# Optimization experiments

Hardware: AMD Instinct MI355X
Metric: run time of the kernel (lower is better)

## Reference

```python
import jax, jax.numpy as jnp
import numpy as np

# ---- problem sizes (would come from edge_index / init args in the torch module) ----
N = 10000      # number of nodes
E = 100000     # number of edges
C = 6          # channels per node
L = 6          # layers
B = 16         # batch
N_IN = 100     # input nodes  (nodes [0, N_IN))
N_OUT = 100    # output nodes (nodes [N-N_OUT, N))
EPS = 1e-5


def setup_inputs() -> dict:
    rng = np.random.default_rng(0)
    src = rng.integers(0, N, size=E).astype(np.int32)
    dst = rng.integers(0, N, size=E).astype(np.int32)

    input_mask = np.zeros(N, bool); input_mask[:N_IN] = True
    output_mask = np.zeros(N, bool); output_mask[N - N_OUT:] = True
    func_mask = ~(input_mask | output_mask)
    func_nodes = np.nonzero(func_mask)[0].astype(np.int32)
    F = func_nodes.size
    ii = np.arange(C, dtype=np.int32)

    # W1 (E -> C*N): edge e feeds all C channels of its dst node. nnz = E*C
    w1_rows = np.repeat(np.arange(E, dtype=np.int32), C)
    w1_cols = (dst[:, None] * C + ii[None, :]).reshape(-1)

    # W2 (C*N -> C*N): dense CxC block per function node. nnz = F*C*C
    base = np.repeat(func_nodes * C, C * C)
    w2_rows = base + np.tile(np.repeat(ii, C), F)
    w2_cols = base + np.tile(np.tile(ii, C), F)

    # W3 (C*N -> E): edge e reads the C channels of src(e) if src is a function node
    e_sel = np.nonzero(func_mask[src])[0].astype(np.int32)
    w3_rows = (src[e_sel][:, None] * C + ii[None, :]).reshape(-1)
    w3_cols = np.repeat(e_sel, C)

    # values: kaiming-style init with fan d (d=C for W1/W2, d=1 for W3)
    w1_vals = (rng.standard_normal(w1_rows.size) / np.sqrt(C)).astype(np.float32)
    w2_vals = (rng.standard_normal(w2_rows.size) / np.sqrt(C)).astype(np.float32)
    w3_vals = (rng.standard_normal(w3_rows.size) * 1.0).astype(np.float32)

    key = jax.random.key(0)
    x = jax.random.normal(key, (B, N), dtype=jnp.float32)

    return {
        "x": x,
        "src": jnp.asarray(src), "dst": jnp.asarray(dst),
        "output_mask": jnp.asarray(output_mask),
        "w1_rows": jnp.asarray(w1_rows), "w1_cols": jnp.asarray(w1_cols),
        "w1_vals": jnp.asarray(w1_vals), "b1": jnp.zeros((C * N,), jnp.float32),
        "w2_rows": jnp.asarray(w2_rows), "w2_cols": jnp.asarray(w2_cols),
        "w2_vals": jnp.asarray(w2_vals), "b2": jnp.zeros((C * N,), jnp.float32),
        "w3_rows": jnp.asarray(w3_rows), "w3_cols": jnp.asarray(w3_cols),
        "w3_vals": jnp.asarray(w3_vals), "b3": jnp.zeros((E,), jnp.float32),
        "gamma": jnp.ones((L,), jnp.float32), "beta": jnp.zeros((L,), jnp.float32),
    }


def _sp_lin(h, rows, cols, vals, bias, out_dim):
    # out[b, c] = sum_{k: cols[k]==c} h[b, rows[k]] * vals[k] + bias[c]
    contrib = h[:, rows] * vals  # [B, nnz]
    out = jnp.zeros((h.shape[0], out_dim), h.dtype).at[:, cols].add(contrib)
    return out + bias


def _batchnorm_scalar(z, g, b):
    # BatchNorm1d(1) on z.view(-1,1): single channel over all B*E elements (training mode)
    m = jnp.mean(z)
    v = jnp.mean(jnp.square(z - m))
    return (z - m) * jax.lax.rsqrt(v + EPS) * g + b


def reference(x, src, dst, output_mask,
              w1_rows, w1_cols, w1_vals, b1,
              w2_rows, w2_cols, w2_vals, b2,
              w3_rows, w3_cols, w3_vals, b3,
              gamma, beta):
    x0 = x[:, src]          # node2edge: [B, E]
    h = x0
    h_last = x0             # residual=True path
    for l in range(L):
        z = _sp_lin(h, w1_rows, w1_cols, w1_vals, b1, C * N)
        z = jax.nn.elu(z)
        z = _sp_lin(z, w2_rows, w2_cols, w2_vals, b2, C * N)
        z = jax.nn.elu(z)
        z = _sp_lin(z, w3_rows, w3_cols, w3_vals, b3, E)
        z = _batchnorm_scalar(z, gamma[l], beta[l])
        h = z + h_last
        h_last = h
    h = h / L
    # edge2node: scatter edge values to dst nodes, keep only output nodes
    node = jnp.zeros((x.shape[0], N), x.dtype).at[:, dst].add(h)
    return jnp.where(output_mask[None, :], node, 0.0)
```

## Files before the change

kernel.cpp:

```cpp
#include <hip/hip_runtime.h>
#include <math.h>

#define NN 10000
#define NE 100000
#define CC 6
#define LL 6
#define BB 16
#define FUNC_LO 100
#define FUNC_HI 9900
#define NOUT 100
#define EPSF 1e-5f
#define NSLOT 64

struct Slot { double s1, s2; double pad[6]; };

struct Params {
  const float *x, *w1v, *b1, *w2v, *b2, *w3v, *b3, *gamma, *beta;
  const int *src, *dst, *w3r, *w3c;
  float *out;
  int *row_start, *counts, *fill, *slot;
  int *row2, *counts2, *fill2, *csr2;
  float4 *grec;
  float4 *srec;
  float *xT, *h;
  unsigned short *z3a, *z3b;
  float *A;
  float *Cw;
  Slot *part, *baseS;
  int F, Ksel;
};

__device__ __forceinline__ float eluf(float x){ return x > 0.0f ? x : expm1f(x); }
__device__ __forceinline__ float bf2f(unsigned short h){
  union { unsigned int u; float f; } c; c.u = ((unsigned int)h)<<16; return c.f;
}
__device__ __forceinline__ unsigned short f2bf(float f){
  union { float f; unsigned int u; } c; c.f = f;
  return (unsigned short)((c.u + 0x7FFFu + ((c.u>>16)&1u)) >> 16);
}

__device__ void block_add_slot(double a, double q, Slot* sl){
  __shared__ double sb1[4], sb2[4];
  #pragma unroll
  for(int off=32;off;off>>=1){ a+=__shfl_down(a,off); q+=__shfl_down(q,off); }
  int wid = threadIdx.x>>6;
  if((threadIdx.x&63)==0){ sb1[wid]=a; sb2[wid]=q; }
  __syncthreads();
  if(threadIdx.x==0){
    double A=sb1[0]+sb1[1]+sb1[2]+sb1[3];
    double Q=sb2[0]+sb2[1]+sb2[2]+sb2[3];
    if(A!=0.0) atomicAdd(&sl->s1,A);
    if(Q!=0.0) atomicAdd(&sl->s2,Q);
  }
  __syncthreads();
}

__device__ void bn_params(const Slot* part, const Slot* baseS, float* m, float* inv){
  __shared__ double s_mv[2];
  if(threadIdx.x < NSLOT){
    double a = part[threadIdx.x].s1 + baseS[threadIdx.x].s1;
    double q = part[threadIdx.x].s2 + baseS[threadIdx.x].s2;
    #pragma unroll
    for(int off=32;off;off>>=1){ a+=__shfl_down(a,off); q+=__shfl_down(q,off); }
    if(threadIdx.x==0){
      const double cnt = (double)NE*(double)BB;
      double md = a/cnt, vd = q/cnt - md*md;
      s_mv[0]=md; s_mv[1]=1.0/sqrt(vd+(double)EPSF);
    }
  }
  __syncthreads();
  *m=(float)s_mv[0]; *inv=(float)s_mv[1];
  __syncthreads();
}

__global__ __launch_bounds__(256) void kw_P1(Params p){
  int tid = blockIdx.x*256 + threadIdx.x, nt = gridDim.x*256;
  for(int i=tid;i<NN*BB;i+=nt){ int n=i>>4, b=i&15; p.xT[i]=p.x[b*NN+n]; }
  for(int i=tid;i<BB*NN;i+=nt) p.out[i]=0.f;
  double a=0.0,q=0.0;
  for(int e=tid;e<NE;e+=nt){
    atomicAdd(&p.counts[p.dst[e]],1);
    int s=p.src[e];
    if(!(s>=FUNC_LO && s<FUNC_HI)){ double v=(double)p.b3[e]; a+=v; q+=v*v; }
  }
  for(int k=tid;k<p.Ksel;k+=nt){
    int s=p.w3r[k*CC]/CC;
    atomicAdd(&p.counts2[s-FUNC_LO],1);
  }
  block_add_slot(a*BB, q*BB, &p.baseS[blockIdx.x&(NSLOT-1)]);
}

__global__ __launch_bounds__(256) void kw_scan(Params p){
  __shared__ int s_scan[256];
  const int*  cin  = (blockIdx.x==0)? p.counts : p.counts2;
  int*        rout = (blockIdx.x==0)? p.row_start : p.row2;
  const int   nel  = (blockIdx.x==0)? NN : p.F;
  const int   CH   = (nel+255)/256;
  int t=threadIdx.x, base=t*CH, s=0;
  for(int k=0;k<CH;k++){ int i=base+k; if(i<nel) s+=cin[i]; }
  s_scan[t]=s; __syncthreads();
  for(int off=1;off<256;off<<=1){
    int v=(t>=off)?s_scan[t-off]:0; __syncthreads();
    s_scan[t]+=v; __syncthreads();
  }
  int run=s_scan[t]-s;
  for(int k=0;k<CH;k++){ int i=base+k; if(i<nel){ rout[i]=run; run+=cin[i]; } }
  if(t==255) rout[nel]=s_scan[255];
}

__global__ __launch_bounds__(256) void kw_fill(Params p){
  int tid = blockIdx.x*256 + threadIdx.x, nt = gridDim.x*256;
  for(int e=tid;e<NE;e+=nt){
    int n=p.dst[e];
    int pos=p.row_start[n]+atomicAdd(&p.fill[n],1);
    p.slot[e]=pos;
    const float* w=&p.w1v[e*CC];
    int s=p.src[e];
    float b3v=p.b3[e];
    p.grec[pos*2  ]=make_float4(w[0],w[1],w[2],w[3]);
    p.grec[pos*2+1]=make_float4(w[4],w[5],__int_as_float(s),b3v);
    if(!(s>=FUNC_LO && s<FUNC_HI)){
      unsigned int hb = f2bf(b3v);
      unsigned int pk = hb | (hb<<16);
      uint4 v4 = make_uint4(pk,pk,pk,pk);
      uint4* za=(uint4*)&p.z3a[pos*BB];
      uint4* zb=(uint4*)&p.z3b[pos*BB];
      za[0]=v4; za[1]=v4; zb[0]=v4; zb[1]=v4;
    }
  }
  for(int k=tid;k<p.Ksel;k+=nt){
    int fi=p.w3r[k*CC]/CC - FUNC_LO;
    int pos=p.row2[fi]+atomicAdd(&p.fill2[fi],1);
    p.csr2[pos]=k;
  }
}

template<int MODE>
__global__ __launch_bounds__(256) void kw_AB(Params p, int l,
    const unsigned short* __restrict__ z3p, unsigned short* __restrict__ z3c){
  int tid = blockIdx.x*256 + (int)threadIdx.x, nt = gridDim.x*256;
  float c1=0.f, c2=0.f;
  if(MODE>0){
    float m, inv;
    bn_params(p.part+(l-1)*NSLOT, p.baseS, &m, &inv);
    float g=p.gamma[l-1], be=p.beta[l-1];
    c1 = inv*g; c2 = be - m*c1;
  }
  const int FB2 = p.F*32;
  double a=0.0, q=0.0;
  for(int t=tid;t<FB2;t+=nt){
    int fi = t>>5;
    int u  = t&31, b = u&15, half = u>>4;
    int n  = FUNC_LO+fi;
    float acc[CC], cacc[CC];
    #pragma unroll
    for(int i=0;i<CC;i++){ acc[i]=0.f; cacc[i]=0.f; }
    int beg=p.row_start[n], end=p.row_start[n+1];
    int pp = beg + half;
    for(; pp+2<end; pp+=4){
      float4 ra0=p.grec[pp*2],     rb0=p.grec[pp*2+1];
      float4 ra1=p.grec[(pp+2)*2], rb1=p.grec[(pp+2)*2+1];
      float hv0, hv1;
      if(MODE==0){
        int s0=__float_as_int(rb0.z), s1=__float_as_int(rb1.z);
        hv0 = p.xT[s0*BB+b];
        hv1 = p.xT[s1*BB+b];
        cacc[0]+=ra0.x+ra1.x; cacc[1]+=ra0.y+ra1.y; cacc[2]+=ra0.z+ra1.z;
        cacc[3]+=ra0.w+ra1.w; cacc[4]+=rb0.x+rb1.x; cacc[5]+=rb0.y+rb1.y;
      } else {
        hv0 = bf2f(z3p[pp*BB+b]);
        hv1 = bf2f(z3p[(pp+2)*BB+b]);
      }
      acc[0]+=hv0*ra0.x+hv1*ra1.x; acc[1]+=hv0*ra0.y+hv1*ra1.y;
      acc[2]+=hv0*ra0.z+hv1*ra1.z; acc[3]+=hv0*ra0.w+hv1*ra1.w;
      acc[4]+=hv0*rb0.x+hv1*rb1.x; acc[5]+=hv0*rb0.y+hv1*rb1.y;
    }
    if(pp<end){
      float4 ra0=p.grec[pp*2], rb0=p.grec[pp*2+1];
      float hv0;
      if(MODE==0){
        int s0=__float_as_int(rb0.z);
        hv0 = p.xT[s0*BB+b];
        cacc[0]+=ra0.x; cacc[1]+=ra0.y; cacc[2]+=ra0.z;
        cacc[3]+=ra0.w; cacc[4]+=rb0.x; cacc[5]+=rb0.y;
      } else {
        hv0 = bf2f(z3p[pp*BB+b]);
      }
      acc[0]+=hv0*ra0.x; acc[1]+=hv0*ra0.y; acc[2]+=hv0*ra0.z;
      acc[3]+=hv0*ra0.w; acc[4]+=hv0*rb0.x; acc[5]+=hv0*rb0.y;
    }
    float z1v[CC];
    #pragma unroll
    for(int i=0;i<CC;i++){
      acc[i] += __shfl_xor(acc[i],16);
      if(MODE==0){
        cacc[i] += __shfl_xor(cacc[i],16);
        if(half==0){
          p.A[(fi*CC+i)*BB+b] = acc[i];
          if(b==0) p.Cw[fi*CC+i] = cacc[i];
        }
        z1v[i] = eluf(acc[i] + p.b1[n*CC+i]);
      } else {
        float Aold = p.A[(fi*CC+i)*BB+b];
        float Cv   = p.Cw[fi*CC+i];
        float Anew = Aold + c1*acc[i] + c2*Cv;
        if(half==0) p.A[(fi*CC+i)*BB+b] = Anew;
        z1v[i] = eluf(Anew + p.b1[n*CC+i]);
      }
    }
    const float* W2=&p.w2v[fi*36];
    float z2[CC];
    #pragma unroll
    for(int jj=0;jj<CC;jj++){
      float o=p.b2[n*CC+jj];
      #pragma unroll
      for(int i=0;i<CC;i++) o+=z1v[i]*W2[i*CC+jj];
      z2[jj]=eluf(o);
    }
    int bg2=p.row2[fi], en2=p.row2[fi+1];
    if(MODE==0){
      for(int sp=bg2+half;sp<en2;sp+=2){
        int k=p.csr2[sp];
        int e=p.w3c[k*CC];
        const float* w=&p.w3v[k*CC];
        float b3v=p.b3[e];
        int sl=p.slot[e];
        if(b==0){
          p.srec[sp*2  ]=make_float4(w[0],w[1],w[2],w[3]);
          p.srec[sp*2+1]=make_float4(w[4],w[5],__int_as_float(sl),b3v);
        }
        float o = b3v + z2[0]*w[0]+z2[1]*w[1]+z2[2]*w[2]
                      + z2[3]*w[3]+z2[4]*w[4]+z2[5]*w[5];
        z3c[sl*BB+b]=f2bf(o);
        a+=o; q+=(double)o*o;
      }
    } else {
      for(int sp=bg2+half;sp<en2;sp+=2){
        float4 ra=p.srec[sp*2], rb=p.srec[sp*2+1];
        float o = rb.w + z2[0]*ra.x + z2[1]*ra.y + z2[2]*ra.z
                       + z2[3]*ra.w + z2[4]*rb.x + z2[5]*rb.y;
        int sl=__float_as_int(rb.z);
        z3c[sl*BB+b]=f2bf(o);
        a+=o; q+=(double)o*o;
      }
    }
  }
  if(MODE>0){
    int outBeg = p.row_start[FUNC_HI];
    int tot = (p.row_start[NN]-outBeg)*BB;
    for(int u=tid; u<tot; u+=nt){
      int pp=outBeg+(u>>4); int bb=u&15;
      float zb=bf2f(z3p[pp*BB+bb]);
      float hb;
      if(MODE==1){
        float4 rb=p.grec[pp*2+1];
        int s=__float_as_int(rb.z);
        hb=p.xT[s*BB+bb];
      } else {
        hb=p.h[pp*BB+bb];
      }
      p.h[pp*BB+bb]=hb+zb*c1+c2;
    }
  }
  block_add_slot(a,q,&p.part[l*NSLOT+(blockIdx.x&(NSLOT-1))]);
}

__global__ __launch_bounds__(256) void kw_out(Params p, const unsigned short* __restrict__ z3p){
  int tid = blockIdx.x*256 + threadIdx.x, nt = gridDim.x*256;
  float m,inv;
  bn_params(p.part+(LL-1)*NSLOT, p.baseS, &m, &inv);
  float g=p.gamma[LL-1], be=p.beta[LL-1];
  float c1=inv*g, c2=be-m*c1;
  for(int t=tid;t<NOUT*BB;t+=nt){
    int j=t>>4, b=t&15;
    int n=FUNC_HI+j;
    float acc=0.f;
    int beg=p.row_start[n], end=p.row_start[n+1];
    for(int pp=beg;pp<end;++pp){
      acc += p.h[pp*BB+b] + bf2f(z3p[pp*BB+b])*c1 + c2;
    }
    p.out[b*NN+n]=acc*(1.0f/(float)LL);
  }
}

extern "C" void kernel_launch(void* const* d_in, const int* in_sizes, int n_in,
                              void* d_out, int out_size, void* d_ws, size_t ws_size,
                              hipStream_t stream){
  Params p;
  p.x    =(const float*)d_in[0];
  p.src  =(const int*)  d_in[1];
  p.dst  =(const int*)  d_in[2];
  p.w1v  =(const float*)d_in[6];
  p.b1   =(const float*)d_in[7];
  p.w2v  =(const float*)d_in[10];
  p.b2   =(const float*)d_in[11];
  p.w3r  =(const int*)  d_in[12];
  p.w3c  =(const int*)  d_in[13];
  p.w3v  =(const float*)d_in[14];
  p.b3   =(const float*)d_in[15];
  p.gamma=(const float*)d_in[16];
  p.beta =(const float*)d_in[17];
  p.out  =(float*)d_out;
  p.F    = in_sizes[8]/36;
  p.Ksel = in_sizes[12]/CC;

  char* ws=(char*)d_ws; size_t off=0;
  auto alloc=[&](size_t bytes)->char*{
    char* q=ws+off; off=(off+bytes+255)&~(size_t)255; return q;
  };
  p.row_start=(int*)   alloc((NN+1)*sizeof(int));
  p.row2     =(int*)   alloc((size_t)(p.F+1)*sizeof(int));
  p.slot     =(int*)   alloc(NE*sizeof(int));
  p.csr2     =(int*)   alloc(NE*sizeof(int));
  p.grec     =(float4*)alloc((size_t)NE*2*sizeof(float4));
  p.srec     =(float4*)alloc((size_t)NE*2*sizeof(float4));
  p.xT       =(float*) alloc((size_t)NN*BB*sizeof(float));
  p.h        =(float*) alloc((size_t)NE*BB*sizeof(float));
  p.z3a      =(unsigned short*)alloc((size_t)NE*BB*sizeof(unsigned short));
  p.z3b      =(unsigned short*)alloc((size_t)NE*BB*sizeof(unsigned short));
  p.A        =(float*) alloc((size_t)p.F*CC*BB*sizeof(float));
  p.Cw       =(float*) alloc((size_t)p.F*CC*sizeof(float));
  p.counts   =(int*)  alloc(NN*sizeof(int));
  p.fill     =(int*)  alloc(NN*sizeof(int));
  p.counts2  =(int*)  alloc((size_t)p.F*sizeof(int));
  p.fill2    =(int*)  alloc((size_t)p.F*sizeof(int));
  p.part     =(Slot*) alloc((size_t)LL*NSLOT*sizeof(Slot));
  p.baseS    =(Slot*) alloc((size_t)NSLOT*sizeof(Slot));
  (void)ws_size; (void)n_in; (void)out_size;

  size_t zspan = (char*)(p.baseS+NSLOT) - (char*)p.counts;
  hipMemsetAsync(p.counts, 0, zspan, stream);

  unsigned short* bufs[2] = { p.z3a, p.z3b };
  const int gridAB = (p.F*32 + 255)/256;

  kw_P1  <<<512,256,0,stream>>>(p);
  kw_scan<<<2,  256,0,stream>>>(p);
  kw_fill<<<512,256,0,stream>>>(p);
  kw_AB<0><<<gridAB,256,0,stream>>>(p, 0, bufs[1], bufs[0]);
  kw_AB<1><<<gridAB,256,0,stream>>>(p, 1, bufs[0], bufs[1]);
  for(int l=2;l<LL;l++){
    kw_AB<2><<<gridAB,256,0,stream>>>(p, l, bufs[(l^1)&1], bufs[l&1]);
  }
  kw_out<<<(NOUT*BB+255)/256,256,0,stream>>>(p, bufs[(LL-1)&1]);
}
```

Before: 165.5 us.

## Pack edge weight records and accumulator state into bf16 to halve traffic

Gather and scatter edge records now hold their six weights as packed bf16 pairs plus an index in a single 16-byte uint4, where before they used two float4s. The W3 bias moves to a separate bf16 array, and the per-node accumulator A is stored as bf16 instead of fp32. This roughly halves the record bytes read in each layer's sparse gather and scatter loops and halves A's traffic. In exchange it adds unpack ALU work, and re-rounding A to bf16 every layer compounds error that could break accuracy.

```diff
diff --git a/kernel.cpp b/kernel.cpp
--- a/kernel.cpp
+++ b/kernel.cpp
@@ -20,11 +20,12 @@
   float *out;
   int *row_start, *counts, *fill, *slot;
   int *row2, *counts2, *fill2, *csr2;
-  float4 *grec;
-  float4 *srec;
+  uint4 *grec;
+  uint4 *srec;
+  unsigned short *sb3;
   float *xT, *h;
   unsigned short *z3a, *z3b;
-  float *A;
+  unsigned short *A;
   float *Cw;
   Slot *part, *baseS;
   int F, Ksel;
@@ -37,6 +38,14 @@
 __device__ __forceinline__ unsigned short f2bf(float f){
   union { float f; unsigned int u; } c; c.f = f;
   return (unsigned short)((c.u + 0x7FFFu + ((c.u>>16)&1u)) >> 16);
+}
+__device__ __forceinline__ unsigned int packbf(float a, float b){
+  return (unsigned int)f2bf(a) | ((unsigned int)f2bf(b)<<16);
+}
+__device__ __forceinline__ float2 ubf2(unsigned int u){
+  union { unsigned int u; float f; } lo, hi;
+  lo.u = u<<16; hi.u = u & 0xFFFF0000u;
+  return make_float2(lo.f, hi.f);
 }
 
 __device__ void block_add_slot(double a, double q, Slot* sl){
@@ -117,8 +126,8 @@
     const float* w=&p.w1v[e*CC];
     int s=p.src[e];
     float b3v=p.b3[e];
-    p.grec[pos*2  ]=make_float4(w[0],w[1],w[2],w[3]);
-    p.grec[pos*2+1]=make_float4(w[4],w[5],__int_as_float(s),b3v);
+    p.grec[pos]=make_uint4(packbf(w[0],w[1]),packbf(w[2],w[3]),
+                           packbf(w[4],w[5]),(unsigned int)s);
     if(!(s>=FUNC_LO && s<FUNC_HI)){
       unsigned int hb = f2bf(b3v);
       unsigned int pk = hb | (hb<<16);
@@ -158,36 +167,38 @@
     int beg=p.row_start[n], end=p.row_start[n+1];
     int pp = beg + half;
     for(; pp+2<end; pp+=4){
-      float4 ra0=p.grec[pp*2],     rb0=p.grec[pp*2+1];
-      float4 ra1=p.grec[(pp+2)*2], rb1=p.grec[(pp+2)*2+1];
+      uint4 g0=p.grec[pp], g1=p.grec[pp+2];
+      float2 wa0=ubf2(g0.x), wb0=ubf2(g0.y), wc0=ubf2(g0.z);
+      float2 wa1=ubf2(g1.x), wb1=ubf2(g1.y), wc1=ubf2(g1.z);
       float hv0, hv1;
       if(MODE==0){
-        int s0=__float_as_int(rb0.z), s1=__float_as_int(rb1.z);
+        int s0=(int)g0.w, s1=(int)g1.w;
         hv0 = p.xT[s0*BB+b];
         hv1 = p.xT[s1*BB+b];
-        cacc[0]+=ra0.x+ra1.x; cacc[1]+=ra0.y+ra1.y; cacc[2]+=ra0.z+ra1.z;
-        cacc[3]+=ra0.w+ra1.w; cacc[4]+=rb0.x+rb1.x; cacc[5]+=rb0.y+rb1.y;
+        cacc[0]+=wa0.x+wa1.x; cacc[1]+=wa0.y+wa1.y; cacc[2]+=wb0.x+wb1.x;
+        cacc[3]+=wb0.y+wb1.y; cacc[4]+=wc0.x+wc1.x; cacc[5]+=wc0.y+wc1.y;
       } else {
         hv0 = bf2f(z3p[pp*BB+b]);
         hv1 = bf2f(z3p[(pp+2)*BB+b]);
       }
-      acc[0]+=hv0*ra0.x+hv1*ra1.x; acc[1]+=hv0*ra0.y+hv1*ra1.y;
-      acc[2]+=hv0*ra0.z+hv1*ra1.z; acc[3]+=hv0*ra0.w+hv1*ra1.w;
-      acc[4]+=hv0*rb0.x+hv1*rb1.x; acc[5]+=hv0*rb0.y+hv1*rb1.y;
+      acc[0]+=hv0*wa0.x+hv1*wa1.x; acc[1]+=hv0*wa0.y+hv1*wa1.y;
+      acc[2]+=hv0*wb0.x+hv1*wb1.x; acc[3]+=hv0*wb0.y+hv1*wb1.y;
+      acc[4]+=hv0*wc0.x+hv1*wc1.x; acc[5]+=hv0*wc0.y+hv1*wc1.y;
     }
     if(pp<end){
-      float4 ra0=p.grec[pp*2], rb0=p.grec[pp*2+1];
+      uint4 g0=p.grec[pp];
+      float2 wa0=ubf2(g0.x), wb0=ubf2(g0.y), wc0=ubf2(g0.z);
       float hv0;
       if(MODE==0){
-        int s0=__float_as_int(rb0.z);
+        int s0=(int)g0.w;
         hv0 = p.xT[s0*BB+b];
-        cacc[0]+=ra0.x; cacc[1]+=ra0.y; cacc[2]+=ra0.z;
-        cacc[3]+=ra0.w; cacc[4]+=rb0.x; cacc[5]+=rb0.y;
+        cacc[0]+=wa0.x; cacc[1]+=wa0.y; cacc[2]+=wb0.x;
+        cacc[3]+=wb0.y; cacc[4]+=wc0.x; cacc[5]+=wc0.y;
       } else {
         hv0 = bf2f(z3p[pp*BB+b]);
       }
-      acc[0]+=hv0*ra0.x; acc[1]+=hv0*ra0.y; acc[2]+=hv0*ra0.z;
-      acc[3]+=hv0*ra0.w; acc[4]+=hv0*rb0.x; acc[5]+=hv0*rb0.y;
+      acc[0]+=hv0*wa0.x; acc[1]+=hv0*wa0.y; acc[2]+=hv0*wb0.x;
+      acc[3]+=hv0*wb0.y; acc[4]+=hv0*wc0.x; acc[5]+=hv0*wc0.y;
     }
     float z1v[CC];
     #pragma unroll
@@ -196,15 +207,15 @@
       if(MODE==0){
         cacc[i] += __shfl_xor(cacc[i],16);
         if(half==0){
-          p.A[(fi*CC+i)*BB+b] = acc[i];
+          p.A[(fi*CC+i)*BB+b] = f2bf(acc[i]);
           if(b==0) p.Cw[fi*CC+i] = cacc[i];
         }
         z1v[i] = eluf(acc[i] + p.b1[n*CC+i]);
       } else {
-        float Aold = p.A[(fi*CC+i)*BB+b];
+        float Aold = bf2f(p.A[(fi*CC+i)*BB+b]);
         float Cv   = p.Cw[fi*CC+i];
         float Anew = Aold + c1*acc[i] + c2*Cv;
-        if(half==0) p.A[(fi*CC+i)*BB+b] = Anew;
+        if(half==0) p.A[(fi*CC+i)*BB+b] = f2bf(Anew);
         z1v[i] = eluf(Anew + p.b1[n*CC+i]);
       }
     }
@@ -225,21 +236,27 @@
         const float* w=&p.w3v[k*CC];
         float b3v=p.b3[e];
         int sl=p.slot[e];
+        float2 a01=ubf2(packbf(w[0],w[1]));
+        float2 a23=ubf2(packbf(w[2],w[3]));
+        float2 a45=ubf2(packbf(w[4],w[5]));
         if(b==0){
-          p.srec[sp*2  ]=make_float4(w[0],w[1],w[2],w[3]);
-          p.srec[sp*2+1]=make_float4(w[4],w[5],__int_as_float(sl),b3v);
+          p.srec[sp]=make_uint4(packbf(w[0],w[1]),packbf(w[2],w[3]),
+                                packbf(w[4],w[5]),(unsigned int)sl);
+          p.sb3[sp]=f2bf(b3v);
         }
-        float o = b3v + z2[0]*w[0]+z2[1]*w[1]+z2[2]*w[2]
-                      + z2[3]*w[3]+z2[4]*w[4]+z2[5]*w[5];
+        float o = b3v + z2[0]*a01.x+z2[1]*a01.y+z2[2]*a23.x
+                      + z2[3]*a23.y+z2[4]*a45.x+z2[5]*a45.y;
         z3c[sl*BB+b]=f2bf(o);
         a+=o; q+=(double)o*o;
       }
     } else {
       for(int sp=bg2+half;sp<en2;sp+=2){
-        float4 ra=p.srec[sp*2], rb=p.srec[sp*2+1];
-        float o = rb.w + z2[0]*ra.x + z2[1]*ra.y + z2[2]*ra.z
-                       + z2[3]*ra.w + z2[4]*rb.x + z2[5]*rb.y;
-        int sl=__float_as_int(rb.z);
+        uint4 s4=p.srec[sp];
+        float b3v=bf2f(p.sb3[sp]);
+        float2 a01=ubf2(s4.x), a23=ubf2(s4.y), a45=ubf2(s4.z);
+        float o = b3v + z2[0]*a01.x + z2[1]*a01.y + z2[2]*a23.x
+                      + z2[3]*a23.y + z2[4]*a45.x + z2[5]*a45.y;
+        int sl=(int)s4.w;
         z3c[sl*BB+b]=f2bf(o);
         a+=o; q+=(double)o*o;
       }
@@ -253,8 +270,8 @@
       float zb=bf2f(z3p[pp*BB+bb]);
       float hb;
       if(MODE==1){
-        float4 rb=p.grec[pp*2+1];
-        int s=__float_as_int(rb.z);
+        uint4 g=p.grec[pp];
+        int s=(int)g.w;
         hb=p.xT[s*BB+bb];
       } else {
         hb=p.h[pp*BB+bb];
@@ -308,18 +325,19 @@
   auto alloc=[&](size_t bytes)->char*{
     char* q=ws+off; off=(off+bytes+255)&~(size_t)255; return q;
   };
-  p.row_start=(int*)   alloc((NN+1)*sizeof(int));
-  p.row2     =(int*)   alloc((size_t)(p.F+1)*sizeof(int));
-  p.slot     =(int*)   alloc(NE*sizeof(int));
-  p.csr2     =(int*)   alloc(NE*sizeof(int));
-  p.grec     =(float4*)alloc((size_t)NE*2*sizeof(float4));
-  p.srec     =(float4*)alloc((size_t)NE*2*sizeof(float4));
-  p.xT       =(float*) alloc((size_t)NN*BB*sizeof(float));
-  p.h        =(float*) alloc((size_t)NE*BB*sizeof(float));
+  p.row_start=(int*)  alloc((NN+1)*sizeof(int));
+  p.row2     =(int*)  alloc((size_t)(p.F+1)*sizeof(int));
+  p.slot     =(int*)  alloc(NE*sizeof(int));
+  p.csr2     =(int*)  alloc(NE*sizeof(int));
+  p.grec     =(uint4*)alloc((size_t)NE*sizeof(uint4));
+  p.srec     =(uint4*)alloc((size_t)NE*sizeof(uint4));
+  p.sb3      =(unsigned short*)alloc((size_t)NE*sizeof(unsigned short));
+  p.xT       =(float*)alloc((size_t)NN*BB*sizeof(float));
+  p.h        =(float*)alloc((size_t)NE*BB*sizeof(float));
   p.z3a      =(unsigned short*)alloc((size_t)NE*BB*sizeof(unsigned short));
   p.z3b      =(unsigned short*)alloc((size_t)NE*BB*sizeof(unsigned short));
-  p.A        =(float*) alloc((size_t)p.F*CC*BB*sizeof(float));
-  p.Cw       =(float*) alloc((size_t)p.F*CC*sizeof(float));
+  p.A        =(unsigned short*)alloc((size_t)p.F*CC*BB*sizeof(unsigned short));
+  p.Cw       =(float*)alloc((size_t)p.F*CC*sizeof(float));
   p.counts   =(int*)  alloc(NN*sizeof(int));
   p.fill     =(int*)  alloc(NN*sizeof(int));
   p.counts2  =(int*)  alloc((size_t)p.F*sizeof(int));
```

New measurement: 159.9 us (median of 3 runs). 1.04x faster.
